# Kernel tuning notes

Measured on AMD Instinct MI355X. Metric: run time of the kernel, lower is better.

## Reference

```python
import jax, jax.numpy as jnp
import numpy as np

B, L, D = 16, 2048, 64

def setup_inputs() -> dict:
    key = jax.random.key(0)
    kq, kk, kv = jax.random.split(key, 3)
    q = jax.random.normal(kq, (B, L, D), dtype=jnp.float32)
    k = jax.random.normal(kk, (B, L, D), dtype=jnp.float32)
    v = jax.random.normal(kv, (B, L, D), dtype=jnp.float32)
    return {"q": q, "k": k, "v": v}

def reference(q, k, v):
    # scores: [B, L_q, L_k] = q @ k^T  (no scale applied, faithful to source)
    scores = jnp.einsum("bqd,bkd->bqk", q, k)
    attention = jax.nn.softmax(scores, axis=2)
    # dropout p=0.0 -> identity
    # source returns (v, attention), NOT the context
    return (v, attention)
```

## Files before the change

### kernel.cpp

```cpp
#include <hip/hip_runtime.h>
#include <hip/hip_bf16.h>

typedef short s16x8 __attribute__((ext_vector_type(8)));
typedef float f32x4 __attribute__((ext_vector_type(4)));

#define B_ 16
#define L_ 2048
#define D_ 64
#define V_ELEMS (B_ * L_ * D_)
#define MFMA16 __builtin_amdgcn_mfma_f32_16x16x32_bf16

__device__ __forceinline__ unsigned rne1(float f) {
    unsigned u = __builtin_bit_cast(unsigned, f);
    return (u + 0x7FFFu + ((u >> 16) & 1u)) >> 16;
}
__device__ __forceinline__ unsigned pack2(float a, float b) {
    return (rne1(a) & 0xFFFFu) | (rne1(b) << 16);
}

__device__ __forceinline__ void split8(float4 a, float4 b, s16x8& hi, s16x8& lo) {
    float f[8] = {a.x, a.y, a.z, a.w, b.x, b.y, b.z, b.w};
    s16x8 h, l;
#pragma unroll
    for (int i = 0; i < 8; ++i) {
        unsigned u = __builtin_bit_cast(unsigned, f[i]);
        h[i] = (short)(u >> 16);
        float lf = f[i] - __builtin_bit_cast(float, u & 0xFFFF0000u);
        l[i] = (short)rne1(lf);
    }
    hi = h; lo = l;
}

__global__ void copy_v_kernel(const float4* __restrict__ v, float4* __restrict__ o) {
    int i = blockIdx.x * blockDim.x + threadIdx.x;
    o[i] = v[i];
}

__global__ void prep_qkv_kernel(const float4* __restrict__ q, const float4* __restrict__ k,
                                const float4* __restrict__ v,
                                uint2* __restrict__ qhi, uint2* __restrict__ qlo,
                                uint2* __restrict__ khi, uint2* __restrict__ klo,
                                float4* __restrict__ o) {
    int i = blockIdx.x * blockDim.x + threadIdx.x;
    o[i] = v[i];
    float4 fq = q[i];
    float4 fk = k[i];
    unsigned u0 = __builtin_bit_cast(unsigned, fq.x), u1 = __builtin_bit_cast(unsigned, fq.y);
    unsigned u2 = __builtin_bit_cast(unsigned, fq.z), u3 = __builtin_bit_cast(unsigned, fq.w);
    qhi[i] = make_uint2((u0 >> 16) | (u1 & 0xFFFF0000u), (u2 >> 16) | (u3 & 0xFFFF0000u));
    qlo[i] = make_uint2(
        pack2(fq.x - __builtin_bit_cast(float, u0 & 0xFFFF0000u),
              fq.y - __builtin_bit_cast(float, u1 & 0xFFFF0000u)),
        pack2(fq.z - __builtin_bit_cast(float, u2 & 0xFFFF0000u),
              fq.w - __builtin_bit_cast(float, u3 & 0xFFFF0000u)));
    u0 = __builtin_bit_cast(unsigned, fk.x); u1 = __builtin_bit_cast(unsigned, fk.y);
    u2 = __builtin_bit_cast(unsigned, fk.z); u3 = __builtin_bit_cast(unsigned, fk.w);
    khi[i] = make_uint2((u0 >> 16) | (u1 & 0xFFFF0000u), (u2 >> 16) | (u3 & 0xFFFF0000u));
    klo[i] = make_uint2(
        pack2(fk.x - __builtin_bit_cast(float, u0 & 0xFFFF0000u),
              fk.y - __builtin_bit_cast(float, u1 & 0xFFFF0000u)),
        pack2(fk.z - __builtin_bit_cast(float, u2 & 0xFFFF0000u),
              fk.w - __builtin_bit_cast(float, u3 & 0xFFFF0000u)));
}

template <bool PRE>
__device__ __forceinline__ void score_tile(
    const float* __restrict__ kf, const ushort* __restrict__ khi,
    const ushort* __restrict__ klo, size_t off,
    const s16x8 (&bhi)[2][2], const s16x8 (&blo)[2][2],
    f32x4& c0, f32x4& c1) {
    s16x8 ahi0, ahi1, alo0, alo1;
    if constexpr (PRE) {
        ahi0 = *(const s16x8*)(khi + off);
        ahi1 = *(const s16x8*)(khi + off + 32);
        alo0 = *(const s16x8*)(klo + off);
        alo1 = *(const s16x8*)(klo + off + 32);
    } else {
        float4 a0 = *(const float4*)(kf + off), a1 = *(const float4*)(kf + off + 4);
        float4 a2 = *(const float4*)(kf + off + 32), a3 = *(const float4*)(kf + off + 36);
        split8(a0, a1, ahi0, alo0);
        split8(a2, a3, ahi1, alo1);
    }
    c0 = (f32x4){0.f, 0.f, 0.f, 0.f};
    c1 = (f32x4){0.f, 0.f, 0.f, 0.f};
    c0 = MFMA16(ahi0, bhi[0][0], c0, 0, 0, 0);
    c0 = MFMA16(ahi1, bhi[0][1], c0, 0, 0, 0);
    c0 = MFMA16(ahi0, blo[0][0], c0, 0, 0, 0);
    c0 = MFMA16(ahi1, blo[0][1], c0, 0, 0, 0);
    c0 = MFMA16(alo0, bhi[0][0], c0, 0, 0, 0);
    c0 = MFMA16(alo1, bhi[0][1], c0, 0, 0, 0);
    c1 = MFMA16(ahi0, bhi[1][0], c1, 0, 0, 0);
    c1 = MFMA16(ahi1, bhi[1][1], c1, 0, 0, 0);
    c1 = MFMA16(ahi0, blo[1][0], c1, 0, 0, 0);
    c1 = MFMA16(ahi1, blo[1][1], c1, 0, 0, 0);
    c1 = MFMA16(alo0, bhi[1][0], c1, 0, 0, 0);
    c1 = MFMA16(alo1, bhi[1][1], c1, 0, 0, 0);
}

template <bool PRE>
__global__ __launch_bounds__(256, 4) void attn_kernel(
    const float* __restrict__ qf, const float* __restrict__ kf,
    const ushort* __restrict__ qhi, const ushort* __restrict__ qlo,
    const ushort* __restrict__ khi, const ushort* __restrict__ klo,
    float* __restrict__ og) {
    const int bid  = ((blockIdx.x & 7) << 7) | (blockIdx.x >> 3);
    const int b    = bid >> 6;
    const int q0   = (bid & 63) << 5;
    const int tid  = threadIdx.x;
    const int wave = tid >> 6;
    const int lane = tid & 63;
    const int nq   = lane & 15;
    const int quad = lane >> 4;

    s16x8 bhi[2][2], blo[2][2];
#pragma unroll
    for (int t = 0; t < 2; ++t) {
        const size_t off = ((size_t)(b * L_ + q0 + t * 16 + nq)) * D_ + quad * 8;
        if constexpr (PRE) {
            bhi[t][0] = *(const s16x8*)(qhi + off);
            bhi[t][1] = *(const s16x8*)(qhi + off + 32);
            blo[t][0] = *(const s16x8*)(qlo + off);
            blo[t][1] = *(const s16x8*)(qlo + off + 32);
        } else {
            float4 a0 = *(const float4*)(qf + off), a1 = *(const float4*)(qf + off + 4);
            float4 a2 = *(const float4*)(qf + off + 32), a3 = *(const float4*)(qf + off + 36);
            split8(a0, a1, bhi[t][0], blo[t][0]);
            split8(a2, a3, bhi[t][1], blo[t][1]);
        }
    }

    const size_t krow0 = (size_t)b * L_ + (size_t)wave * 512 + nq;

    float s0 = 0.0f, s1 = 0.0f;
#pragma unroll 2
    for (int t = 0; t < 32; ++t) {
        const size_t off = (krow0 + (size_t)t * 16) * D_ + quad * 8;
        f32x4 c0, c1;
        score_tile<PRE>(kf, khi, klo, off, bhi, blo, c0, c1);
        s0 += (__expf(c0[0]) + __expf(c0[1])) + (__expf(c0[2]) + __expf(c0[3]));
        s1 += (__expf(c1[0]) + __expf(c1[1])) + (__expf(c1[2]) + __expf(c1[3]));
    }

    s0 += __shfl_xor(s0, 16); s0 += __shfl_xor(s0, 32);
    s1 += __shfl_xor(s1, 16); s1 += __shfl_xor(s1, 32);
    __shared__ float wsum[4][2][16];
    if (lane < 16) { wsum[wave][0][lane] = s0; wsum[wave][1][lane] = s1; }
    __syncthreads();
    const float inv0 = 1.0f / ((wsum[0][0][nq] + wsum[1][0][nq]) + (wsum[2][0][nq] + wsum[3][0][nq]));
    const float inv1 = 1.0f / ((wsum[0][1][nq] + wsum[1][1][nq]) + (wsum[2][1][nq] + wsum[3][1][nq]));

    float* op0 = og + ((size_t)(b * L_ + q0 + nq)) * L_ + wave * 512 + quad * 4;
    float* op1 = op0 + (size_t)16 * L_;
#pragma unroll 2
    for (int t = 0; t < 32; ++t) {
        const size_t off = (krow0 + (size_t)t * 16) * D_ + quad * 8;
        f32x4 c0, c1;
        score_tile<PRE>(kf, khi, klo, off, bhi, blo, c0, c1);
        f32x4 w0, w1;
        w0[0] = __expf(c0[0]) * inv0; w0[1] = __expf(c0[1]) * inv0;
        w0[2] = __expf(c0[2]) * inv0; w0[3] = __expf(c0[3]) * inv0;
        w1[0] = __expf(c1[0]) * inv1; w1[1] = __expf(c1[1]) * inv1;
        w1[2] = __expf(c1[2]) * inv1; w1[3] = __expf(c1[3]) * inv1;
        __builtin_nontemporal_store(w0, (f32x4*)(op0 + (size_t)t * 16));
        __builtin_nontemporal_store(w1, (f32x4*)(op1 + (size_t)t * 16));
    }
}

extern "C" void kernel_launch(void* const* d_in, const int* in_sizes, int n_in,
                              void* d_out, int out_size, void* d_ws, size_t ws_size,
                              hipStream_t stream) {
    const float* q = (const float*)d_in[0];
    const float* k = (const float*)d_in[1];
    const float* v = (const float*)d_in[2];
    float* out = (float*)d_out;

    float* att = out + (size_t)V_ELEMS;
    const size_t plane = (size_t)V_ELEMS;
    const size_t need  = 4 * plane * sizeof(ushort);
    ushort* qhi = (ushort*)d_ws;
    ushort* qlo = qhi + plane;
    ushort* khi = qlo + plane;
    ushort* klo = khi + plane;

    if (ws_size >= need) {
        prep_qkv_kernel<<<dim3(V_ELEMS / 4 / 256), dim3(256), 0, stream>>>(
            (const float4*)q, (const float4*)k, (const float4*)v,
            (uint2*)qhi, (uint2*)qlo, (uint2*)khi, (uint2*)klo, (float4*)out);
        attn_kernel<true><<<dim3(B_ * (L_ / 32)), dim3(256), 0, stream>>>(
            q, k, qhi, qlo, khi, klo, att);
    } else {
        copy_v_kernel<<<dim3(V_ELEMS / 4 / 256), dim3(256), 0, stream>>>(
            (const float4*)v, (float4*)out);
        attn_kernel<false><<<dim3(B_ * (L_ / 32)), dim3(256), 0, stream>>>(
            q, k, qhi, qlo, khi, klo, att);
    }
}
```

Measured before the change: 389.4 us.

## Cache exp scores in registers as bf16 and widen blocks to 1024 threads

Each wave now handles 128 keys instead of 512, with 16 waves per block. Each wave computes the QK^T tiles once, keeping the exponentials packed as bf16 in registers. After the block-wide row sum, it rescales and stores them, instead of recomputing the scores in a second pass. K tiles are software-prefetched one step ahead. This removes half the MFMA and exp work, but it rounds the stored probabilities to bf16 precision and raises register pressure and block size.

```diff
diff --git a/kernel.cpp b/kernel.cpp
--- a/kernel.cpp
+++ b/kernel.cpp
@@ -16,6 +16,11 @@
 }
 __device__ __forceinline__ unsigned pack2(float a, float b) {
     return (rne1(a) & 0xFFFFu) | (rne1(b) << 16);
+}
+__device__ __forceinline__ unsigned cvtpk(float a, float b) {
+    unsigned r;
+    asm("v_cvt_pk_bf16_f32 %0, %1, %2" : "=v"(r) : "v"(a), "v"(b));
+    return r;
 }
 
 __device__ __forceinline__ void split8(float4 a, float4 b, s16x8& hi, s16x8& lo) {
@@ -63,42 +68,17 @@
               fk.w - __builtin_bit_cast(float, u3 & 0xFFFF0000u)));
 }
 
+__device__ __forceinline__ void store4nt(float* p, unsigned u0, unsigned u1, float inv) {
+    f32x4 w;
+    w[0] = __builtin_bit_cast(float, u0 << 16) * inv;
+    w[1] = __builtin_bit_cast(float, u0 & 0xFFFF0000u) * inv;
+    w[2] = __builtin_bit_cast(float, u1 << 16) * inv;
+    w[3] = __builtin_bit_cast(float, u1 & 0xFFFF0000u) * inv;
+    __builtin_nontemporal_store(w, (f32x4*)p);
+}
+
 template <bool PRE>
-__device__ __forceinline__ void score_tile(
-    const float* __restrict__ kf, const ushort* __restrict__ khi,
-    const ushort* __restrict__ klo, size_t off,
-    const s16x8 (&bhi)[2][2], const s16x8 (&blo)[2][2],
-    f32x4& c0, f32x4& c1) {
-    s16x8 ahi0, ahi1, alo0, alo1;
-    if constexpr (PRE) {
-        ahi0 = *(const s16x8*)(khi + off);
-        ahi1 = *(const s16x8*)(khi + off + 32);
-        alo0 = *(const s16x8*)(klo + off);
-        alo1 = *(const s16x8*)(klo + off + 32);
-    } else {
-        float4 a0 = *(const float4*)(kf + off), a1 = *(const float4*)(kf + off + 4);
-        float4 a2 = *(const float4*)(kf + off + 32), a3 = *(const float4*)(kf + off + 36);
-        split8(a0, a1, ahi0, alo0);
-        split8(a2, a3, ahi1, alo1);
-    }
-    c0 = (f32x4){0.f, 0.f, 0.f, 0.f};
-    c1 = (f32x4){0.f, 0.f, 0.f, 0.f};
-    c0 = MFMA16(ahi0, bhi[0][0], c0, 0, 0, 0);
-    c0 = MFMA16(ahi1, bhi[0][1], c0, 0, 0, 0);
-    c0 = MFMA16(ahi0, blo[0][0], c0, 0, 0, 0);
-    c0 = MFMA16(ahi1, blo[0][1], c0, 0, 0, 0);
-    c0 = MFMA16(alo0, bhi[0][0], c0, 0, 0, 0);
-    c0 = MFMA16(alo1, bhi[0][1], c0, 0, 0, 0);
-    c1 = MFMA16(ahi0, bhi[1][0], c1, 0, 0, 0);
-    c1 = MFMA16(ahi1, bhi[1][1], c1, 0, 0, 0);
-    c1 = MFMA16(ahi0, blo[1][0], c1, 0, 0, 0);
-    c1 = MFMA16(ahi1, blo[1][1], c1, 0, 0, 0);
-    c1 = MFMA16(alo0, bhi[1][0], c1, 0, 0, 0);
-    c1 = MFMA16(alo1, bhi[1][1], c1, 0, 0, 0);
-}
-
-template <bool PRE>
-__global__ __launch_bounds__(256, 4) void attn_kernel(
+__global__ __launch_bounds__(1024, 4) void attn_kernel(
     const float* __restrict__ qf, const float* __restrict__ kf,
     const ushort* __restrict__ qhi, const ushort* __restrict__ qlo,
     const ushort* __restrict__ khi, const ushort* __restrict__ klo,
@@ -129,40 +109,84 @@
         }
     }
 
-    const size_t krow0 = (size_t)b * L_ + (size_t)wave * 512 + nq;
+    const size_t kbase = ((size_t)(b * L_ + wave * 128 + nq)) * D_ + quad * 8;
+    const size_t tstep = (size_t)16 * D_;
 
     float s0 = 0.0f, s1 = 0.0f;
-#pragma unroll 2
-    for (int t = 0; t < 32; ++t) {
-        const size_t off = (krow0 + (size_t)t * 16) * D_ + quad * 8;
-        f32x4 c0, c1;
-        score_tile<PRE>(kf, khi, klo, off, bhi, blo, c0, c1);
-        s0 += (__expf(c0[0]) + __expf(c0[1])) + (__expf(c0[2]) + __expf(c0[3]));
-        s1 += (__expf(c1[0]) + __expf(c1[1])) + (__expf(c1[2]) + __expf(c1[3]));
+    unsigned pk0[16], pk1[16];
+
+    s16x8 ah0, ah1, al0, al1;
+    if constexpr (PRE) {
+        ah0 = *(const s16x8*)(khi + kbase);
+        ah1 = *(const s16x8*)(khi + kbase + 32);
+        al0 = *(const s16x8*)(klo + kbase);
+        al1 = *(const s16x8*)(klo + kbase + 32);
+    } else {
+        float4 a0 = *(const float4*)(kf + kbase), a1 = *(const float4*)(kf + kbase + 4);
+        float4 a2 = *(const float4*)(kf + kbase + 32), a3 = *(const float4*)(kf + kbase + 36);
+        split8(a0, a1, ah0, al0);
+        split8(a2, a3, ah1, al1);
+    }
+
+#pragma unroll
+    for (int t = 0; t < 8; ++t) {
+        const size_t noff = kbase + (size_t)((t + 1) & 7) * tstep;
+        s16x8 nh0, nh1, nl0, nl1;
+        if constexpr (PRE) {
+            nh0 = *(const s16x8*)(khi + noff);
+            nh1 = *(const s16x8*)(khi + noff + 32);
+            nl0 = *(const s16x8*)(klo + noff);
+            nl1 = *(const s16x8*)(klo + noff + 32);
+        } else {
+            float4 a0 = *(const float4*)(kf + noff), a1 = *(const float4*)(kf + noff + 4);
+            float4 a2 = *(const float4*)(kf + noff + 32), a3 = *(const float4*)(kf + noff + 36);
+            split8(a0, a1, nh0, nl0);
+            split8(a2, a3, nh1, nl1);
+        }
+
+        f32x4 c0 = {0.f, 0.f, 0.f, 0.f}, c1 = {0.f, 0.f, 0.f, 0.f};
+        c0 = MFMA16(ah0, bhi[0][0], c0, 0, 0, 0);
+        c1 = MFMA16(ah0, bhi[1][0], c1, 0, 0, 0);
+        c0 = MFMA16(ah1, bhi[0][1], c0, 0, 0, 0);
+        c1 = MFMA16(ah1, bhi[1][1], c1, 0, 0, 0);
+        c0 = MFMA16(ah0, blo[0][0], c0, 0, 0, 0);
+        c1 = MFMA16(ah0, blo[1][0], c1, 0, 0, 0);
+        c0 = MFMA16(ah1, blo[0][1], c0, 0, 0, 0);
+        c1 = MFMA16(ah1, blo[1][1], c1, 0, 0, 0);
+        c0 = MFMA16(al0, bhi[0][0], c0, 0, 0, 0);
+        c1 = MFMA16(al0, bhi[1][0], c1, 0, 0, 0);
+        c0 = MFMA16(al1, bhi[0][1], c0, 0, 0, 0);
+        c1 = MFMA16(al1, bhi[1][1], c1, 0, 0, 0);
+
+        float e0 = __expf(c0[0]), e1 = __expf(c0[1]), e2 = __expf(c0[2]), e3 = __expf(c0[3]);
+        s0 += (e0 + e1) + (e2 + e3);
+        pk0[2 * t]     = cvtpk(e0, e1);
+        pk0[2 * t + 1] = cvtpk(e2, e3);
+        float g0 = __expf(c1[0]), g1 = __expf(c1[1]), g2 = __expf(c1[2]), g3 = __expf(c1[3]);
+        s1 += (g0 + g1) + (g2 + g3);
+        pk1[2 * t]     = cvtpk(g0, g1);
+        pk1[2 * t + 1] = cvtpk(g2, g3);
+
+        ah0 = nh0; ah1 = nh1; al0 = nl0; al1 = nl1;
     }
 
     s0 += __shfl_xor(s0, 16); s0 += __shfl_xor(s0, 32);
     s1 += __shfl_xor(s1, 16); s1 += __shfl_xor(s1, 32);
-    __shared__ float wsum[4][2][16];
+    __shared__ float wsum[16][2][16];
     if (lane < 16) { wsum[wave][0][lane] = s0; wsum[wave][1][lane] = s1; }
     __syncthreads();
-    const float inv0 = 1.0f / ((wsum[0][0][nq] + wsum[1][0][nq]) + (wsum[2][0][nq] + wsum[3][0][nq]));
-    const float inv1 = 1.0f / ((wsum[0][1][nq] + wsum[1][1][nq]) + (wsum[2][1][nq] + wsum[3][1][nq]));
-
-    float* op0 = og + ((size_t)(b * L_ + q0 + nq)) * L_ + wave * 512 + quad * 4;
+    float t0 = 0.f, t1 = 0.f;
+#pragma unroll
+    for (int w = 0; w < 16; ++w) { t0 += wsum[w][0][nq]; t1 += wsum[w][1][nq]; }
+    const float inv0 = 1.0f / t0;
+    const float inv1 = 1.0f / t1;
+
+    float* op0 = og + ((size_t)(b * L_ + q0 + nq)) * L_ + wave * 128 + quad * 4;
     float* op1 = op0 + (size_t)16 * L_;
-#pragma unroll 2
-    for (int t = 0; t < 32; ++t) {
-        const size_t off = (krow0 + (size_t)t * 16) * D_ + quad * 8;
-        f32x4 c0, c1;
-        score_tile<PRE>(kf, khi, klo, off, bhi, blo, c0, c1);
-        f32x4 w0, w1;
-        w0[0] = __expf(c0[0]) * inv0; w0[1] = __expf(c0[1]) * inv0;
-        w0[2] = __expf(c0[2]) * inv0; w0[3] = __expf(c0[3]) * inv0;
-        w1[0] = __expf(c1[0]) * inv1; w1[1] = __expf(c1[1]) * inv1;
-        w1[2] = __expf(c1[2]) * inv1; w1[3] = __expf(c1[3]) * inv1;
-        __builtin_nontemporal_store(w0, (f32x4*)(op0 + (size_t)t * 16));
-        __builtin_nontemporal_store(w1, (f32x4*)(op1 + (size_t)t * 16));
+#pragma unroll
+    for (int t = 0; t < 8; ++t) {
+        store4nt(op0 + t * 16, pk0[2 * t], pk0[2 * t + 1], inv0);
+        store4nt(op1 + t * 16, pk1[2 * t], pk1[2 * t + 1], inv1);
     }
 }
 
@@ -186,12 +210,12 @@
         prep_qkv_kernel<<<dim3(V_ELEMS / 4 / 256), dim3(256), 0, stream>>>(
             (const float4*)q, (const float4*)k, (const float4*)v,
             (uint2*)qhi, (uint2*)qlo, (uint2*)khi, (uint2*)klo, (float4*)out);
-        attn_kernel<true><<<dim3(B_ * (L_ / 32)), dim3(256), 0, stream>>>(
+        attn_kernel<true><<<dim3(B_ * (L_ / 32)), dim3(1024), 0, stream>>>(
             q, k, qhi, qlo, khi, klo, att);
     } else {
         copy_v_kernel<<<dim3(V_ELEMS / 4 / 256), dim3(256), 0, stream>>>(
             (const float4*)v, (float4*)out);
-        attn_kernel<false><<<dim3(B_ * (L_ / 32)), dim3(256), 0, stream>>>(
+        attn_kernel<false><<<dim3(B_ * (L_ / 32)), dim3(1024), 0, stream>>>(
             q, k, qhi, qlo, khi, klo, att);
     }
 }
```

New measurement: 385.7 us. Within noise of the previous version (-0.9%).
